# Kernel optimization log

Hardware: AMD Instinct MI355X
Metric: run time of the kernel (lower is better)

Reference implementation:

```python
import jax, jax.numpy as jnp
import numpy as np

DIM = 768
NUM_HEADS = 12
HEAD_DIM = DIM // NUM_HEADS
ORDER_H = 8
RENORM = True
B, N = 4, 1024


def setup_inputs() -> dict:
    key = jax.random.key(0)
    ks = jax.random.split(key, 8)
    return {
        "x": jax.random.normal(ks[0], (B, N, DIM), dtype=jnp.float32),
        "qkv_w": jax.random.normal(ks[1], (3 * DIM, DIM), dtype=jnp.float32) * (DIM ** -0.5),
        "qkv_b": jax.random.normal(ks[2], (3 * DIM,), dtype=jnp.float32) * 0.02,
        "proj_w": jax.random.normal(ks[3], (DIM, DIM), dtype=jnp.float32) * (DIM ** -0.5),
        "proj_b": jax.random.normal(ks[4], (DIM,), dtype=jnp.float32) * 0.02,
        "lamb": jax.random.normal(ks[5], (NUM_HEADS,), dtype=jnp.float32) * 0.1,
        "gamma": 1.0 + jax.random.normal(ks[6], (NUM_HEADS,), dtype=jnp.float32) * 0.1,
        "delta": jax.random.normal(ks[7], (NUM_HEADS,), dtype=jnp.float32) * 0.1,
    }


def reference(x, qkv_w, qkv_b, proj_w, proj_b, lamb, gamma, delta):
    Bx, Nx, C = x.shape
    scale = HEAD_DIM ** -0.5
    # qkv: [B,N,3C] -> [3,B,H,N,hd]
    qkv = (x @ qkv_w.T + qkv_b).reshape(Bx, Nx, 3, NUM_HEADS, HEAD_DIM)
    qkv = jnp.transpose(qkv, (2, 0, 3, 1, 4))
    q, k, v = qkv[0], qkv[1], qkv[2]
    attn = jax.nn.softmax(jnp.einsum("bhid,bhjd->bhij", q, k) * scale, axis=-1)
    I = jnp.eye(Nx, dtype=attn.dtype)
    # GFSA high-order term: (h-1)*(A - I)@A + A
    high = (ORDER_H - 1) * jnp.einsum("bhik,bhkj->bhij", attn - I, attn) + attn
    beta_ = lamb[None, :, None, None]
    gamma_ = gamma[None, :, None, None]
    delta_ = delta[None, :, None, None]
    attn = delta_ * I + gamma_ * attn + beta_ * high
    if RENORM:
        attn = jnp.maximum(attn, 0.0)
        attn = attn / (attn.sum(axis=-1, keepdims=True) + 1e-9)
    out = jnp.einsum("bhij,bhjd->bhid", attn, v)  # [B,H,N,hd]
    out = jnp.transpose(out, (0, 2, 1, 3)).reshape(Bx, Nx, C)
    return out @ proj_w.T + proj_b
```

## Files before the change

kernel.cpp:

```cpp
#include <hip/hip_runtime.h>
#include <hip/hip_bf16.h>

#define DIMC 768
#define NH 12
#define HD 64
#define BB 4
#define NN 1024
#define BHT 48
#define QKVC 2304

typedef unsigned short u16;
typedef __attribute__((ext_vector_type(4))) unsigned short u16x4;
typedef __attribute__((ext_vector_type(8))) unsigned short u16x8;
typedef __attribute__((ext_vector_type(8))) short s16x8;
typedef __attribute__((ext_vector_type(4))) float f32x4;

#define GLD16(g, l) __builtin_amdgcn_global_load_lds( \
    (__attribute__((address_space(1))) void*)(g),     \
    (__attribute__((address_space(3))) void*)(l), 16, 0, 0)

__device__ __forceinline__ u16 f2bf(float f) {
    unsigned u = __float_as_uint(f);
    return (u16)((u + 0x7FFF + ((u >> 16) & 1)) >> 16);
}
__device__ __forceinline__ float bf2f(u16 v) {
    return __uint_as_float(((unsigned)v) << 16);
}
struct bfp { u16 h, l; };
__device__ __forceinline__ bfp splitf(float f) {
    bfp r;
    r.h = f2bf(f);
    r.l = f2bf(f - bf2f(r.h));
    return r;
}

__device__ __forceinline__ int swz_linear() {
    const int nwg = gridDim.x * gridDim.y * gridDim.z;
    const int L = blockIdx.x + gridDim.x * (blockIdx.y + gridDim.y * blockIdx.z);
    return (L & 7) * (nwg >> 3) + (L >> 3);
}

__global__ __launch_bounds__(256) void split_f2b(
    const float* __restrict__ src, u16* __restrict__ hi, u16* __restrict__ lo,
    int n4)
{
    int idx = blockIdx.x * 256 + threadIdx.x;
    if (idx >= n4) return;
    float4 v = *(const float4*)&src[idx * 4];
    u16x4 h, l;
    bfp s;
    s = splitf(v.x); h[0] = s.h; l[0] = s.l;
    s = splitf(v.y); h[1] = s.h; l[1] = s.l;
    s = splitf(v.z); h[2] = s.h; l[2] = s.l;
    s = splitf(v.w); h[3] = s.h; l[3] = s.l;
    *(u16x4*)&hi[idx * 4] = h;
    *(u16x4*)&lo[idx * 4] = l;
}

__global__ __launch_bounds__(256) void gemm3_mfma(
    int Mrows, int Nout, int K,
    const u16* __restrict__ Ahp, const u16* __restrict__ Alp,
    const u16* __restrict__ Bhp, const u16* __restrict__ Blp,
    const float* __restrict__ bias, float* __restrict__ C)
{
    __shared__ alignas(16) u16 sAh[128 * 32], sAl[128 * 32], sBh[128 * 32], sBl[128 * 32];
    const int tid = threadIdx.x;
    const int W = swz_linear();
    const int j0 = (W % gridDim.x) * 128, i0 = (W / gridDim.x) * 128;
    const int w = tid >> 6, l = tid & 63;
    const int wr = w >> 1, wc = w & 1;
    const int l15 = l & 15, kb4 = l >> 4;
    const int lrow = l >> 2, lch = (l & 3) * 8;

    f32x4 acc[4][4];
    const f32x4 zero = {0.f, 0.f, 0.f, 0.f};
#pragma unroll
    for (int a = 0; a < 4; ++a)
#pragma unroll
        for (int b = 0; b < 4; ++b) acc[a][b] = zero;

    for (int k0 = 0; k0 < K; k0 += 32) {
#pragma unroll
        for (int t = 0; t < 2; ++t) {
            const int r = w * 32 + t * 16;
            const size_t ar = (size_t)(i0 + r + lrow) * K + k0 + lch;
            const size_t br = (size_t)(j0 + r + lrow) * K + k0 + lch;
            GLD16(&Ahp[ar], &sAh[r * 32]);
            GLD16(&Alp[ar], &sAl[r * 32]);
            GLD16(&Bhp[br], &sBh[r * 32]);
            GLD16(&Blp[br], &sBl[r * 32]);
        }
        __syncthreads();

        s16x8 ah[4], al[4], bh[4], bl[4];
#pragma unroll
        for (int f = 0; f < 4; ++f) {
            const int ao = (wr * 64 + f * 16 + l15) * 32 + kb4 * 8;
            const int bo = (wc * 64 + f * 16 + l15) * 32 + kb4 * 8;
            ah[f] = *(const s16x8*)&sAh[ao];
            al[f] = *(const s16x8*)&sAl[ao];
            bh[f] = *(const s16x8*)&sBh[bo];
            bl[f] = *(const s16x8*)&sBl[bo];
        }
#pragma unroll
        for (int fr = 0; fr < 4; ++fr)
#pragma unroll
            for (int fc = 0; fc < 4; ++fc) {
                acc[fr][fc] = __builtin_amdgcn_mfma_f32_16x16x32_bf16(
                    ah[fr], bh[fc], acc[fr][fc], 0, 0, 0);
                acc[fr][fc] = __builtin_amdgcn_mfma_f32_16x16x32_bf16(
                    ah[fr], bl[fc], acc[fr][fc], 0, 0, 0);
                acc[fr][fc] = __builtin_amdgcn_mfma_f32_16x16x32_bf16(
                    al[fr], bh[fc], acc[fr][fc], 0, 0, 0);
            }
        __syncthreads();
    }

#pragma unroll
    for (int fr = 0; fr < 4; ++fr)
#pragma unroll
        for (int r = 0; r < 4; ++r) {
            const int gi = i0 + wr * 64 + fr * 16 + kb4 * 4 + r;
#pragma unroll
            for (int fc = 0; fc < 4; ++fc) {
                const int gj = j0 + wc * 64 + fc * 16 + l15;
                C[(size_t)gi * Nout + gj] = acc[fr][fc][r] + bias[gj];
            }
        }
}

__global__ __launch_bounds__(256) void qkv_fused_mfma(
    const u16* __restrict__ Ahp, const u16* __restrict__ Alp,
    const u16* __restrict__ Bhp, const u16* __restrict__ Blp,
    const float* __restrict__ bias,
    u16* __restrict__ qh, u16* __restrict__ ql,
    u16* __restrict__ kh, u16* __restrict__ kl,
    u16* __restrict__ vth, u16* __restrict__ vtl)
{
    __shared__ alignas(16) u16 sAh[128 * 32], sAl[128 * 32], sBh[128 * 32], sBl[128 * 32];
    const int tid = threadIdx.x;
    const int W = swz_linear();
    const int j0 = (W % gridDim.x) * 128, i0 = (W / gridDim.x) * 128;
    const int w = tid >> 6, l = tid & 63;
    const int wr = w >> 1, wc = w & 1;
    const int l15 = l & 15, kb4 = l >> 4;
    const int lrow = l >> 2, lch = (l & 3) * 8;
    const int K = DIMC;

    f32x4 acc[4][4];
    const f32x4 zero = {0.f, 0.f, 0.f, 0.f};
#pragma unroll
    for (int a = 0; a < 4; ++a)
#pragma unroll
        for (int b = 0; b < 4; ++b) acc[a][b] = zero;

    for (int k0 = 0; k0 < K; k0 += 32) {
#pragma unroll
        for (int t = 0; t < 2; ++t) {
            const int r = w * 32 + t * 16;
            const size_t ar = (size_t)(i0 + r + lrow) * K + k0 + lch;
            const size_t br = (size_t)(j0 + r + lrow) * K + k0 + lch;
            GLD16(&Ahp[ar], &sAh[r * 32]);
            GLD16(&Alp[ar], &sAl[r * 32]);
            GLD16(&Bhp[br], &sBh[r * 32]);
            GLD16(&Blp[br], &sBl[r * 32]);
        }
        __syncthreads();

        s16x8 ah[4], al[4], bh[4], bl[4];
#pragma unroll
        for (int f = 0; f < 4; ++f) {
            const int ao = (wr * 64 + f * 16 + l15) * 32 + kb4 * 8;
            const int bo = (wc * 64 + f * 16 + l15) * 32 + kb4 * 8;
            ah[f] = *(const s16x8*)&sAh[ao];
            al[f] = *(const s16x8*)&sAl[ao];
            bh[f] = *(const s16x8*)&sBh[bo];
            bl[f] = *(const s16x8*)&sBl[bo];
        }
#pragma unroll
        for (int fr = 0; fr < 4; ++fr)
#pragma unroll
            for (int fc = 0; fc < 4; ++fc) {
                acc[fr][fc] = __builtin_amdgcn_mfma_f32_16x16x32_bf16(
                    ah[fr], bh[fc], acc[fr][fc], 0, 0, 0);
                acc[fr][fc] = __builtin_amdgcn_mfma_f32_16x16x32_bf16(
                    ah[fr], bl[fc], acc[fr][fc], 0, 0, 0);
                acc[fr][fc] = __builtin_amdgcn_mfma_f32_16x16x32_bf16(
                    al[fr], bh[fc], acc[fr][fc], 0, 0, 0);
            }
        __syncthreads();
    }

    const int part = j0 / DIMC;
    const int hbase = (j0 % DIMC) >> 6;
    const int h = hbase + wc;

#pragma unroll
    for (int fr = 0; fr < 4; ++fr) {
        const int rowbase = i0 + wr * 64 + fr * 16 + kb4 * 4;
        const int b = rowbase >> 10;
        const int n0 = rowbase & 1023;
        const int bh = b * NH + h;
#pragma unroll
        for (int fc = 0; fc < 4; ++fc) {
            const int gj = j0 + wc * 64 + fc * 16 + l15;
            const float bv = bias[gj];
            const int d = fc * 16 + l15;
            if (part == 0) {
#pragma unroll
                for (int r = 0; r < 4; ++r) {
                    bfp s = splitf((acc[fr][fc][r] + bv) * 0.125f);
                    const size_t o = ((size_t)bh * NN + n0 + r) * HD + d;
                    qh[o] = s.h; ql[o] = s.l;
                }
            } else if (part == 1) {
#pragma unroll
                for (int r = 0; r < 4; ++r) {
                    bfp s = splitf(acc[fr][fc][r] + bv);
                    const size_t o = ((size_t)bh * NN + n0 + r) * HD + d;
                    kh[o] = s.h; kl[o] = s.l;
                }
            } else {
                u16x4 hv, lv;
#pragma unroll
                for (int r = 0; r < 4; ++r) {
                    bfp s = splitf(acc[fr][fc][r] + bv);
                    hv[r] = s.h; lv[r] = s.l;
                }
                const size_t o = ((size_t)bh * HD + d) * NN + n0;
                *(u16x4*)&vth[o] = hv;
                *(u16x4*)&vtl[o] = lv;
            }
        }
    }
}

__global__ __launch_bounds__(256) void qk_mfma(
    const u16* __restrict__ qh, const u16* __restrict__ ql,
    const u16* __restrict__ kh, const u16* __restrict__ kl,
    float* __restrict__ Sb, int h0)
{
    __shared__ alignas(16) u16 sAh[128 * 32], sAl[128 * 32], sBh[128 * 32], sBl[128 * 32];
    const int tid = threadIdx.x;
    const int W = swz_linear();
    const int bhl = W >> 6;
    const int ib = W & 63;
    const int j0 = (ib & 7) * 128, i0 = (ib >> 3) * 128;
    const int bh = h0 + bhl;
    const int w = tid >> 6, l = tid & 63;
    const int wr = w >> 1, wc = w & 1;
    const int l15 = l & 15, kb4 = l >> 4;
    const int lrow = l >> 2, lch = (l & 3) * 8;

    f32x4 acc[4][4];
    const f32x4 zero = {0.f, 0.f, 0.f, 0.f};
#pragma unroll
    for (int a = 0; a < 4; ++a)
#pragma unroll
        for (int b = 0; b < 4; ++b) acc[a][b] = zero;

    for (int k0 = 0; k0 < HD; k0 += 32) {
#pragma unroll
        for (int t = 0; t < 2; ++t) {
            const int r = w * 32 + t * 16;
            const size_t ar = ((size_t)bh * NN + i0 + r + lrow) * HD + k0 + lch;
            const size_t br = ((size_t)bh * NN + j0 + r + lrow) * HD + k0 + lch;
            GLD16(&qh[ar], &sAh[r * 32]);
            GLD16(&ql[ar], &sAl[r * 32]);
            GLD16(&kh[br], &sBh[r * 32]);
            GLD16(&kl[br], &sBl[r * 32]);
        }
        __syncthreads();

        s16x8 ah[4], al[4], bh[4], bl[4];
#pragma unroll
        for (int f = 0; f < 4; ++f) {
            const int ao = (wr * 64 + f * 16 + l15) * 32 + kb4 * 8;
            const int bo = (wc * 64 + f * 16 + l15) * 32 + kb4 * 8;
            ah[f] = *(const s16x8*)&sAh[ao];
            al[f] = *(const s16x8*)&sAl[ao];
            bh[f] = *(const s16x8*)&sBh[bo];
            bl[f] = *(const s16x8*)&sBl[bo];
        }
#pragma unroll
        for (int fr = 0; fr < 4; ++fr)
#pragma unroll
            for (int fc = 0; fc < 4; ++fc) {
                acc[fr][fc] = __builtin_amdgcn_mfma_f32_16x16x32_bf16(
                    ah[fr], bh[fc], acc[fr][fc], 0, 0, 0);
                acc[fr][fc] = __builtin_amdgcn_mfma_f32_16x16x32_bf16(
                    ah[fr], bl[fc], acc[fr][fc], 0, 0, 0);
                acc[fr][fc] = __builtin_amdgcn_mfma_f32_16x16x32_bf16(
                    al[fr], bh[fc], acc[fr][fc], 0, 0, 0);
            }
        __syncthreads();
    }

    float* Sh = Sb + (size_t)bhl * NN * NN;
#pragma unroll
    for (int fr = 0; fr < 4; ++fr)
#pragma unroll
        for (int r = 0; r < 4; ++r) {
            const int gi = i0 + wr * 64 + fr * 16 + kb4 * 4 + r;
#pragma unroll
            for (int fc = 0; fc < 4; ++fc) {
                const int gj = j0 + wc * 64 + fc * 16 + l15;
                Sh[(size_t)gi * NN + gj] = acc[fr][fc][r];
            }
        }
}

__global__ __launch_bounds__(256) void softmax_b(
    const float* __restrict__ Sb, u16* __restrict__ Abf)
{
    const int row = blockIdx.x;
    const float* p = Sb + (size_t)row * NN;
    u16* q = Abf + (size_t)row * NN;
    const int tid = threadIdx.x;
    __shared__ float redm[4], reds[4];

    float4 v = *(const float4*)&p[tid * 4];
    float m = fmaxf(fmaxf(v.x, v.y), fmaxf(v.z, v.w));
#pragma unroll
    for (int off = 32; off >= 1; off >>= 1) m = fmaxf(m, __shfl_xor(m, off));
    if ((tid & 63) == 0) redm[tid >> 6] = m;
    __syncthreads();
    m = fmaxf(fmaxf(redm[0], redm[1]), fmaxf(redm[2], redm[3]));

    v.x = expf(v.x - m); v.y = expf(v.y - m);
    v.z = expf(v.z - m); v.w = expf(v.w - m);
    float s = v.x + v.y + v.z + v.w;
#pragma unroll
    for (int off = 32; off >= 1; off >>= 1) s += __shfl_xor(s, off);
    if ((tid & 63) == 0) reds[tid >> 6] = s;
    __syncthreads();
    s = reds[0] + reds[1] + reds[2] + reds[3];

    const float inv = 1.0f / s;
    u16x4 o;
    o[0] = f2bf(v.x * inv); o[1] = f2bf(v.y * inv);
    o[2] = f2bf(v.z * inv); o[3] = f2bf(v.w * inv);
    *(u16x4*)&q[tid * 4] = o;
}

__global__ __launch_bounds__(256) void mpow_mfma(
    const u16* __restrict__ Abf, u16* __restrict__ Mb,
    const float* __restrict__ lamb, const float* __restrict__ gamma,
    const float* __restrict__ delta, int h0)
{
    __shared__ alignas(16) u16 sA[128 * 32], sB[128 * 32];
    const int tid = threadIdx.x;
    const int W = swz_linear();
    const int bz = W >> 6;
    const int ib = W & 63;
    const int j0 = (ib & 7) * 128, i0 = (ib >> 3) * 128;
    const int h = (h0 + bz) % NH;
    const u16* Ah = Abf + (size_t)bz * NN * NN;

    const int w = tid >> 6, l = tid & 63;
    const int wr = w >> 1, wc = w & 1;
    const int l15 = l & 15, kb4 = l >> 4;
    const int lrow = l >> 2, lch = (l & 3) * 8;
    const int kr = tid & 31;
    const int jc = (tid >> 5) * 16;

    f32x4 acc[4][4];
    const f32x4 zero = {0.f, 0.f, 0.f, 0.f};
#pragma unroll
    for (int a = 0; a < 4; ++a)
#pragma unroll
        for (int b = 0; b < 4; ++b) acc[a][b] = zero;

    for (int k0 = 0; k0 < NN; k0 += 32) {
#pragma unroll
        for (int t = 0; t < 2; ++t) {
            const int r = w * 32 + t * 16;
            GLD16(&Ah[(size_t)(i0 + r + lrow) * NN + k0 + lch], &sA[r * 32]);
        }
        {
            const u16* arow = &Ah[(size_t)(k0 + kr) * NN + j0 + jc];
            u16x8 b0 = *(const u16x8*)arow;
            u16x8 b1 = *(const u16x8*)(arow + 8);
#pragma unroll
            for (int e = 0; e < 8; ++e) {
                sB[(jc + e) * 32 + kr]     = b0[e];
                sB[(jc + 8 + e) * 32 + kr] = b1[e];
            }
        }
        __syncthreads();

        s16x8 af[4], bf[4];
#pragma unroll
        for (int f = 0; f < 4; ++f) {
            af[f] = *(const s16x8*)&sA[(wr * 64 + f * 16 + l15) * 32 + kb4 * 8];
            bf[f] = *(const s16x8*)&sB[(wc * 64 + f * 16 + l15) * 32 + kb4 * 8];
        }
#pragma unroll
        for (int fr = 0; fr < 4; ++fr)
#pragma unroll
            for (int fc = 0; fc < 4; ++fc)
                acc[fr][fc] = __builtin_amdgcn_mfma_f32_16x16x32_bf16(
                    af[fr], bf[fc], acc[fr][fc], 0, 0, 0);
        __syncthreads();
    }

    const float lam = lamb[h];
    const float c1 = gamma[h] - 6.0f * lam;
    const float c2 = 7.0f * lam;
    const float del = delta[h];
    u16* Mh = Mb + (size_t)bz * NN * NN;

#pragma unroll
    for (int fr = 0; fr < 4; ++fr)
#pragma unroll
        for (int r = 0; r < 4; ++r) {
            const int gi = i0 + wr * 64 + fr * 16 + kb4 * 4 + r;
#pragma unroll
            for (int fc = 0; fc < 4; ++fc) {
                const int gj = j0 + wc * 64 + fc * 16 + l15;
                const float a = bf2f(Ah[(size_t)gi * NN + gj]);
                float m = c2 * acc[fr][fc][r] + c1 * a + (gi == gj ? del : 0.f);
                m = fmaxf(m, 0.f);
                Mh[(size_t)gi * NN + gj] = f2bf(m);
            }
        }
}

__global__ __launch_bounds__(256) void pv_mfma(
    const u16* __restrict__ Mb,
    const u16* __restrict__ vth, const u16* __restrict__ vtl,
    u16* __restrict__ aoh, u16* __restrict__ aol, int h0)
{
    __shared__ alignas(16) u16 sM[128 * 32], sVh[64 * 32], sVl[64 * 32];
    const int tid = threadIdx.x;
    const int W = swz_linear();
    const int bhl = W >> 3;
    const int i0 = (W & 7) * 128;
    const int bh = h0 + bhl;
    const int b = bh / NH, h = bh % NH;
    const u16* Mh = Mb + (size_t)bhl * NN * NN;
    const u16* vhb = vth + (size_t)bh * HD * NN;
    const u16* vlb = vtl + (size_t)bh * HD * NN;

    const int w = tid >> 6, l = tid & 63;
    const int l15 = l & 15, kb4 = l >> 4;
    const int lrow = l >> 2, lch = (l & 3) * 8;

    f32x4 acc[2][4], accs[2];
    const f32x4 zero = {0.f, 0.f, 0.f, 0.f};
#pragma unroll
    for (int a = 0; a < 2; ++a) {
#pragma unroll
        for (int c = 0; c < 4; ++c) acc[a][c] = zero;
        accs[a] = zero;
    }
    s16x8 ones;
#pragma unroll
    for (int e = 0; e < 8; ++e) ones[e] = (short)0x3F80;

    for (int k0 = 0; k0 < NN; k0 += 32) {
#pragma unroll
        for (int t = 0; t < 2; ++t) {
            const int r = w * 32 + t * 16;
            GLD16(&Mh[(size_t)(i0 + r + lrow) * NN + k0 + lch], &sM[r * 32]);
        }
        {
            const int r = w * 16;
            const size_t vr = (size_t)(r + lrow) * NN + k0 + lch;
            GLD16(&vhb[vr], &sVh[r * 32]);
            GLD16(&vlb[vr], &sVl[r * 32]);
        }
        __syncthreads();

        s16x8 af[2], bh[4], bl[4];
#pragma unroll
        for (int f = 0; f < 2; ++f)
            af[f] = *(const s16x8*)&sM[(w * 32 + f * 16 + l15) * 32 + kb4 * 8];
#pragma unroll
        for (int f = 0; f < 4; ++f) {
            bh[f] = *(const s16x8*)&sVh[(f * 16 + l15) * 32 + kb4 * 8];
            bl[f] = *(const s16x8*)&sVl[(f * 16 + l15) * 32 + kb4 * 8];
        }
#pragma unroll
        for (int fr = 0; fr < 2; ++fr) {
#pragma unroll
            for (int fc = 0; fc < 4; ++fc) {
                acc[fr][fc] = __builtin_amdgcn_mfma_f32_16x16x32_bf16(
                    af[fr], bh[fc], acc[fr][fc], 0, 0, 0);
                acc[fr][fc] = __builtin_amdgcn_mfma_f32_16x16x32_bf16(
                    af[fr], bl[fc], acc[fr][fc], 0, 0, 0);
            }
            accs[fr] = __builtin_amdgcn_mfma_f32_16x16x32_bf16(
                af[fr], ones, accs[fr], 0, 0, 0);
        }
        __syncthreads();
    }

#pragma unroll
    for (int fr = 0; fr < 2; ++fr)
#pragma unroll
        for (int r = 0; r < 4; ++r) {
            const int gi = i0 + w * 32 + fr * 16 + kb4 * 4 + r;
            const float inv = 1.0f / (accs[fr][r] + 1e-9f);
            const size_t ob = (size_t)(b * NN + gi) * DIMC + h * HD;
#pragma unroll
            for (int fc = 0; fc < 4; ++fc) {
                const int gd = fc * 16 + l15;
                bfp s = splitf(acc[fr][fc][r] * inv);
                aoh[ob + gd] = s.h;
                aol[ob + gd] = s.l;
            }
        }
}

extern "C" void kernel_launch(void* const* d_in, const int* in_sizes, int n_in,
                              void* d_out, int out_size, void* d_ws, size_t ws_size,
                              hipStream_t stream)
{
    const float* x      = (const float*)d_in[0];
    const float* qkv_w  = (const float*)d_in[1];
    const float* qkv_b  = (const float*)d_in[2];
    const float* proj_w = (const float*)d_in[3];
    const float* proj_b = (const float*)d_in[4];
    const float* lamb   = (const float*)d_in[5];
    const float* gamma  = (const float*)d_in[6];
    const float* delta  = (const float*)d_in[7];

    char* p = (char*)d_ws;
    u16* xh  = (u16*)p;                     p += (size_t)4096 * DIMC * 2;
    u16* xl  = (u16*)p;                     p += (size_t)4096 * DIMC * 2;
    u16* wh  = (u16*)p;                     p += (size_t)QKVC * DIMC * 2;
    u16* wl  = (u16*)p;                     p += (size_t)QKVC * DIMC * 2;
    u16* pwh = (u16*)p;                     p += (size_t)DIMC * DIMC * 2;
    u16* pwl = (u16*)p;                     p += (size_t)DIMC * DIMC * 2;
    u16* qh  = (u16*)p;                     p += (size_t)BHT * NN * HD * 2;
    u16* ql  = (u16*)p;                     p += (size_t)BHT * NN * HD * 2;
    u16* kh  = (u16*)p;                     p += (size_t)BHT * NN * HD * 2;
    u16* kl  = (u16*)p;                     p += (size_t)BHT * NN * HD * 2;
    u16* vth = (u16*)p;                     p += (size_t)BHT * HD * NN * 2;
    u16* vtl = (u16*)p;                     p += (size_t)BHT * HD * NN * 2;
    u16* aoh = (u16*)p;                     p += (size_t)4096 * DIMC * 2;
    u16* aol = (u16*)p;                     p += (size_t)4096 * DIMC * 2;
    const size_t fixed = (size_t)(p - (char*)d_ws);

    const size_t perh = (size_t)NN * NN * 4 + (size_t)NN * NN * 2;
    static const int choices[] = {48, 24, 16, 12, 8, 6, 4, 3, 2, 1};
    int CH = 1;
    for (int ci = 0; ci < 10; ++ci) {
        int c = choices[ci];
        if (fixed + (size_t)c * perh <= ws_size) { CH = c; break; }
    }

    float* Sb = (float*)p;                  p += (size_t)CH * NN * NN * 4;
    u16* Abf  = (u16*)p;                    p += (size_t)CH * NN * NN * 2;
    u16* Mb   = (u16*)Sb;

    split_f2b<<<dim3((4096 * DIMC / 4 + 255) / 256), 256, 0, stream>>>(x, xh, xl, 4096 * DIMC / 4);
    split_f2b<<<dim3((QKVC * DIMC / 4 + 255) / 256), 256, 0, stream>>>(qkv_w, wh, wl, QKVC * DIMC / 4);
    split_f2b<<<dim3((DIMC * DIMC / 4 + 255) / 256), 256, 0, stream>>>(proj_w, pwh, pwl, DIMC * DIMC / 4);

    qkv_fused_mfma<<<dim3(QKVC / 128, 4096 / 128), 256, 0, stream>>>(
        xh, xl, wh, wl, qkv_b, qh, ql, kh, kl, vth, vtl);

    for (int h0 = 0; h0 < BHT; h0 += CH) {
        qk_mfma<<<dim3(8, 8, CH), 256, 0, stream>>>(qh, ql, kh, kl, Sb, h0);
        softmax_b<<<dim3(CH * NN), 256, 0, stream>>>(Sb, Abf);
        mpow_mfma<<<dim3(8, 8, CH), 256, 0, stream>>>(
            Abf, Mb, lamb, gamma, delta, h0);
        pv_mfma<<<dim3(8, CH), 256, 0, stream>>>(Mb, vth, vtl, aoh, aol, h0);
    }

    gemm3_mfma<<<dim3(DIMC / 128, 4096 / 128), 256, 0, stream>>>(
        4096, DIMC, DIMC, aoh, aol, pwh, pwl, proj_b, (float*)d_out);
}
```

Baseline: 439.4 us.

## Store V untransposed, transpose in pv LDS; one-wave-per-row softmax

```diff
diff --git a/kernel.cpp b/kernel.cpp
--- a/kernel.cpp
+++ b/kernel.cpp
@@ -135,7 +135,7 @@
     const float* __restrict__ bias,
     u16* __restrict__ qh, u16* __restrict__ ql,
     u16* __restrict__ kh, u16* __restrict__ kl,
-    u16* __restrict__ vth, u16* __restrict__ vtl)
+    u16* __restrict__ vh, u16* __restrict__ vl)
 {
     __shared__ alignas(16) u16 sAh[128 * 32], sAl[128 * 32], sBh[128 * 32], sBl[128 * 32];
     const int tid = threadIdx.x;
@@ -194,6 +194,9 @@
     const int part = j0 / DIMC;
     const int hbase = (j0 % DIMC) >> 6;
     const int h = hbase + wc;
+    u16* dsth = (part == 0) ? qh : (part == 1) ? kh : vh;
+    u16* dstl = (part == 0) ? ql : (part == 1) ? kl : vl;
+    const float sc = (part == 0) ? 0.125f : 1.0f;
 
 #pragma unroll
     for (int fr = 0; fr < 4; ++fr) {
@@ -206,30 +209,11 @@
             const int gj = j0 + wc * 64 + fc * 16 + l15;
             const float bv = bias[gj];
             const int d = fc * 16 + l15;
-            if (part == 0) {
-#pragma unroll
-                for (int r = 0; r < 4; ++r) {
-                    bfp s = splitf((acc[fr][fc][r] + bv) * 0.125f);
-                    const size_t o = ((size_t)bh * NN + n0 + r) * HD + d;
-                    qh[o] = s.h; ql[o] = s.l;
-                }
-            } else if (part == 1) {
-#pragma unroll
-                for (int r = 0; r < 4; ++r) {
-                    bfp s = splitf(acc[fr][fc][r] + bv);
-                    const size_t o = ((size_t)bh * NN + n0 + r) * HD + d;
-                    kh[o] = s.h; kl[o] = s.l;
-                }
-            } else {
-                u16x4 hv, lv;
-#pragma unroll
-                for (int r = 0; r < 4; ++r) {
-                    bfp s = splitf(acc[fr][fc][r] + bv);
-                    hv[r] = s.h; lv[r] = s.l;
-                }
-                const size_t o = ((size_t)bh * HD + d) * NN + n0;
-                *(u16x4*)&vth[o] = hv;
-                *(u16x4*)&vtl[o] = lv;
+#pragma unroll
+            for (int r = 0; r < 4; ++r) {
+                bfp s = splitf((acc[fr][fc][r] + bv) * sc);
+                const size_t o = ((size_t)bh * NN + n0 + r) * HD + d;
+                dsth[o] = s.h; dstl[o] = s.l;
             }
         }
     }
@@ -310,37 +294,42 @@
         }
 }
 
-__global__ __launch_bounds__(256) void softmax_b(
+__global__ __launch_bounds__(256) void softmax_w(
     const float* __restrict__ Sb, u16* __restrict__ Abf)
 {
-    const int row = blockIdx.x;
+    const int w = threadIdx.x >> 6, l = threadIdx.x & 63;
+    const int row = blockIdx.x * 4 + w;
     const float* p = Sb + (size_t)row * NN;
     u16* q = Abf + (size_t)row * NN;
-    const int tid = threadIdx.x;
-    __shared__ float redm[4], reds[4];
-
-    float4 v = *(const float4*)&p[tid * 4];
-    float m = fmaxf(fmaxf(v.x, v.y), fmaxf(v.z, v.w));
+
+    float4 v[4];
+    float m = -1e30f;
+#pragma unroll
+    for (int c = 0; c < 4; ++c) {
+        v[c] = *(const float4*)&p[c * 256 + l * 4];
+        m = fmaxf(m, fmaxf(fmaxf(v[c].x, v[c].y), fmaxf(v[c].z, v[c].w)));
+    }
 #pragma unroll
     for (int off = 32; off >= 1; off >>= 1) m = fmaxf(m, __shfl_xor(m, off));
-    if ((tid & 63) == 0) redm[tid >> 6] = m;
-    __syncthreads();
-    m = fmaxf(fmaxf(redm[0], redm[1]), fmaxf(redm[2], redm[3]));
-
-    v.x = expf(v.x - m); v.y = expf(v.y - m);
-    v.z = expf(v.z - m); v.w = expf(v.w - m);
-    float s = v.x + v.y + v.z + v.w;
+
+    float s = 0.f;
+#pragma unroll
+    for (int c = 0; c < 4; ++c) {
+        v[c].x = expf(v[c].x - m); v[c].y = expf(v[c].y - m);
+        v[c].z = expf(v[c].z - m); v[c].w = expf(v[c].w - m);
+        s += v[c].x + v[c].y + v[c].z + v[c].w;
+    }
 #pragma unroll
     for (int off = 32; off >= 1; off >>= 1) s += __shfl_xor(s, off);
-    if ((tid & 63) == 0) reds[tid >> 6] = s;
-    __syncthreads();
-    s = reds[0] + reds[1] + reds[2] + reds[3];
 
     const float inv = 1.0f / s;
-    u16x4 o;
-    o[0] = f2bf(v.x * inv); o[1] = f2bf(v.y * inv);
-    o[2] = f2bf(v.z * inv); o[3] = f2bf(v.w * inv);
-    *(u16x4*)&q[tid * 4] = o;
+#pragma unroll
+    for (int c = 0; c < 4; ++c) {
+        u16x4 o;
+        o[0] = f2bf(v[c].x * inv); o[1] = f2bf(v[c].y * inv);
+        o[2] = f2bf(v[c].z * inv); o[3] = f2bf(v[c].w * inv);
+        *(u16x4*)&q[c * 256 + l * 4] = o;
+    }
 }
 
 __global__ __launch_bounds__(256) void mpow_mfma(
@@ -428,10 +417,11 @@
 
 __global__ __launch_bounds__(256) void pv_mfma(
     const u16* __restrict__ Mb,
-    const u16* __restrict__ vth, const u16* __restrict__ vtl,
+    const u16* __restrict__ vh, const u16* __restrict__ vl,
     u16* __restrict__ aoh, u16* __restrict__ aol, int h0)
 {
-    __shared__ alignas(16) u16 sM[128 * 32], sVh[64 * 32], sVl[64 * 32];
+    __shared__ alignas(16) u16 sM[128 * 32];
+    __shared__ alignas(16) u16 sVh[64 * 40], sVl[64 * 40];
     const int tid = threadIdx.x;
     const int W = swz_linear();
     const int bhl = W >> 3;
@@ -439,12 +429,13 @@
     const int bh = h0 + bhl;
     const int b = bh / NH, h = bh % NH;
     const u16* Mh = Mb + (size_t)bhl * NN * NN;
-    const u16* vhb = vth + (size_t)bh * HD * NN;
-    const u16* vlb = vtl + (size_t)bh * HD * NN;
+    const u16* vhb = vh + (size_t)bh * NN * HD;
+    const u16* vlb = vl + (size_t)bh * NN * HD;
 
     const int w = tid >> 6, l = tid & 63;
     const int l15 = l & 15, kb4 = l >> 4;
     const int lrow = l >> 2, lch = (l & 3) * 8;
+    const int nr = tid >> 3, dc = (tid & 7) * 8;
 
     f32x4 acc[2][4], accs[2];
     const f32x4 zero = {0.f, 0.f, 0.f, 0.f};
@@ -465,10 +456,14 @@
             GLD16(&Mh[(size_t)(i0 + r + lrow) * NN + k0 + lch], &sM[r * 32]);
         }
         {
-            const int r = w * 16;
-            const size_t vr = (size_t)(r + lrow) * NN + k0 + lch;
-            GLD16(&vhb[vr], &sVh[r * 32]);
-            GLD16(&vlb[vr], &sVl[r * 32]);
+            const size_t vr = (size_t)(k0 + nr) * HD + dc;
+            u16x8 hv = *(const u16x8*)&vhb[vr];
+            u16x8 lv = *(const u16x8*)&vlb[vr];
+#pragma unroll
+            for (int e = 0; e < 8; ++e) {
+                sVh[(dc + e) * 40 + nr] = hv[e];
+                sVl[(dc + e) * 40 + nr] = lv[e];
+            }
         }
         __syncthreads();
 
@@ -478,8 +473,8 @@
             af[f] = *(const s16x8*)&sM[(w * 32 + f * 16 + l15) * 32 + kb4 * 8];
 #pragma unroll
         for (int f = 0; f < 4; ++f) {
-            bh[f] = *(const s16x8*)&sVh[(f * 16 + l15) * 32 + kb4 * 8];
-            bl[f] = *(const s16x8*)&sVl[(f * 16 + l15) * 32 + kb4 * 8];
+            bh[f] = *(const s16x8*)&sVh[(f * 16 + l15) * 40 + kb4 * 8];
+            bl[f] = *(const s16x8*)&sVl[(f * 16 + l15) * 40 + kb4 * 8];
         }
 #pragma unroll
         for (int fr = 0; fr < 2; ++fr) {
@@ -537,8 +532,8 @@
     u16* ql  = (u16*)p;                     p += (size_t)BHT * NN * HD * 2;
     u16* kh  = (u16*)p;                     p += (size_t)BHT * NN * HD * 2;
     u16* kl  = (u16*)p;                     p += (size_t)BHT * NN * HD * 2;
-    u16* vth = (u16*)p;                     p += (size_t)BHT * HD * NN * 2;
-    u16* vtl = (u16*)p;                     p += (size_t)BHT * HD * NN * 2;
+    u16* vh  = (u16*)p;                     p += (size_t)BHT * NN * HD * 2;
+    u16* vl  = (u16*)p;                     p += (size_t)BHT * NN * HD * 2;
     u16* aoh = (u16*)p;                     p += (size_t)4096 * DIMC * 2;
     u16* aol = (u16*)p;                     p += (size_t)4096 * DIMC * 2;
     const size_t fixed = (size_t)(p - (char*)d_ws);
@@ -560,14 +555,14 @@
     split_f2b<<<dim3((DIMC * DIMC / 4 + 255) / 256), 256, 0, stream>>>(proj_w, pwh, pwl, DIMC * DIMC / 4);
 
     qkv_fused_mfma<<<dim3(QKVC / 128, 4096 / 128), 256, 0, stream>>>(
-        xh, xl, wh, wl, qkv_b, qh, ql, kh, kl, vth, vtl);
+        xh, xl, wh, wl, qkv_b, qh, ql, kh, kl, vh, vl);
 
     for (int h0 = 0; h0 < BHT; h0 += CH) {
         qk_mfma<<<dim3(8, 8, CH), 256, 0, stream>>>(qh, ql, kh, kl, Sb, h0);
-        softmax_b<<<dim3(CH * NN), 256, 0, stream>>>(Sb, Abf);
+        softmax_w<<<dim3(CH * NN / 4), 256, 0, stream>>>(Sb, Abf);
         mpow_mfma<<<dim3(8, 8, CH), 256, 0, stream>>>(
             Abf, Mb, lamb, gamma, delta, h0);
-        pv_mfma<<<dim3(8, CH), 256, 0, stream>>>(Mb, vth, vtl, aoh, aol, h0);
+        pv_mfma<<<dim3(8, CH), 256, 0, stream>>>(Mb, vh, vl, aoh, aol, h0);
     }
 
     gemm3_mfma<<<dim3(DIMC / 128, 4096 / 128), 256, 0, stream>>>(
```

After: 459.1 us. 1.04x slower.
